# Kernel tuning notes

Hardware: AMD Instinct MI355X
Metric: run time of the kernel (lower is better)

Reference implementation:

```python
import jax, jax.numpy as jnp
import numpy as np

EPS = 1e-5
POOL_R, POOL_T, SCALE = 5, 7, 0.125  # pool_r, pool_t, 1/pool_stride


def conv_bn_relu(x, W, b, gamma, beta, pad):
    # Conv2d(bias) + BatchNorm2d (training-mode batch stats, biased var) + ReLU
    y = jax.lax.conv_general_dilated(x, W, (1, 1), [(pad, pad), (pad, pad)],
                                     dimension_numbers=('NCHW', 'OIHW', 'NCHW'))
    y = y + b[None, :, None, None]
    mean = y.mean(axis=(0, 2, 3))
    var = y.var(axis=(0, 2, 3))
    y = (y - mean[None, :, None, None]) * jax.lax.rsqrt(var + EPS)[None, :, None, None]
    y = y * gamma[None, :, None, None] + beta[None, :, None, None]
    return jax.nn.relu(y)


def linear_bn_relu(x, W, b, gamma, beta):
    # LinearBlock: Linear + BatchNorm (over batch dim) + ReLU
    y = x @ W.T + b
    mean = y.mean(axis=0)
    var = y.var(axis=0)
    y = (y - mean) * jax.lax.rsqrt(var + EPS) * gamma + beta
    return jax.nn.relu(y)


def _hat_int(x):
    # Antiderivative of the triangular (bilinear) hat kernel at offset x.
    u = jnp.clip(x, -1.0, 1.0)
    return jnp.where(u <= 0, 0.5 * (1.0 + u) ** 2, 0.5 + u - 0.5 * u ** 2)


def prroi_pool(feat, rois, ph, pw, scale):
    # Exact PrRoIPool2D. feat: [B,C,H,W]; rois: [B,N,4] xyxy in image coords.
    # Bilinear interp is a sum of separable hat kernels at integer grid points, so the
    # exact bin integral factorizes into per-axis hat-integral weights Wx, Wy.
    B, C, H, W = feat.shape
    x1, y1, x2, y2 = [rois[..., i] * scale for i in range(4)]
    bw = (x2 - x1) / pw   # [B,N]
    bh = (y2 - y1) / ph
    qx = jnp.arange(pw, dtype=feat.dtype)
    qy = jnp.arange(ph, dtype=feat.dtype)
    xs_lo = x1[..., None] + qx * bw[..., None]   # [B,N,Pw]
    ys_lo = y1[..., None] + qy * bh[..., None]   # [B,N,Ph]
    gw = jnp.arange(W, dtype=feat.dtype)
    gh = jnp.arange(H, dtype=feat.dtype)
    Wx = _hat_int(xs_lo[..., None] + bw[..., None, None] - gw) - _hat_int(xs_lo[..., None] - gw)  # [B,N,Pw,W]
    Wy = _hat_int(ys_lo[..., None] + bh[..., None, None] - gh) - _hat_int(ys_lo[..., None] - gh)  # [B,N,Ph,H]
    out = jnp.einsum('bchw,bnph,bnqw->bncpq', feat, Wy, Wx)
    area = (bw * bh)[:, :, None, None, None]
    return jnp.where(area > 0, out / jnp.maximum(area, 1e-12), 0.0)  # [B,N,C,Ph,Pw]


def _forward(feat1, feat2, bb1, proposals2,
             w_c1r, b_c1r, g_c1r, be_c1r,
             w_c1t, b_c1t, g_c1t, be_c1t,
             w_c2t, b_c2t, g_c2t, be_c2t,
             w_f1r, b_f1r, g_f1r, be_f1r,
             w_f2r, b_f2r, g_f2r, be_f2r,
             w_f1rt, b_f1rt, g_f1rt, be_f1rt,
             w_f2rt, b_f2rt, g_f2rt, be_f2rt,
             w_iou, b_iou):
    S = feat2.shape[0]
    N = proposals2.shape[2]
    # --- get_modulation ---
    c3_r = conv_bn_relu(feat1, w_c1r, b_c1r, g_c1r, be_c1r, 1)
    bb = bb1[0]  # [S,4] xywh -> xyxy
    roi_r = jnp.concatenate([bb[:, :2], bb[:, :2] + bb[:, 2:4]], axis=1)[:, None, :]
    pooled_r = prroi_pool(c3_r, roi_r, POOL_R, POOL_R, SCALE)[:, 0]   # [S,256,5,5]
    m = conv_bn_relu(pooled_r, w_f1r, b_f1r, g_f1r, be_f1r, 0)        # [S,1024,1,1]
    m = conv_bn_relu(m, w_f2r, b_f2r, g_f2r, be_f2r, 0)               # [S,256,1,1]
    modulation = m.reshape(S, -1)                                     # [S,256]
    # --- get_iou_feat ---
    c3_t = conv_bn_relu(conv_bn_relu(feat2, w_c1t, b_c1t, g_c1t, be_c1t, 1),
                        w_c2t, b_c2t, g_c2t, be_c2t, 1)
    # --- predict_iou ---
    c3_t_att = c3_t * modulation[:, :, None, None]
    props = proposals2[0]  # [S,N,4] xywh -> xyxy
    rois_t = jnp.concatenate([props[..., :2], props[..., :2] + props[..., 2:4]], axis=-1)
    pooled_t = prroi_pool(c3_t_att, rois_t, POOL_T, POOL_T, SCALE)    # [S,N,256,7,7]
    x = pooled_t.reshape(S * N, -1)
    x = linear_bn_relu(x, w_f1rt, b_f1rt, g_f1rt, be_f1rt)
    x = linear_bn_relu(x, w_f2rt, b_f2rt, g_f2rt, be_f2rt)
    iou = x @ w_iou.T + b_iou
    return iou.reshape(1, S, N)  # (num_images, num_sequences, num_proposals)


def setup_inputs() -> dict:
    key = jax.random.key(0)
    ks = jax.random.split(key, 8)
    S, C, Hf, Wf, N = 64, 256, 36, 36, 16
    inp = {}
    inp['feat1'] = jax.random.normal(ks[0], (S, C, Hf, Wf), jnp.float32)
    inp['feat2'] = jax.random.normal(ks[1], (S, C, Hf, Wf), jnp.float32)
    xy1 = jax.random.uniform(ks[2], (1, S, 2), minval=20.0, maxval=180.0)
    wh1 = jax.random.uniform(ks[3], (1, S, 2), minval=40.0, maxval=100.0)
    inp['bb1'] = jnp.concatenate([xy1, wh1], axis=-1).astype(jnp.float32)
    xy2 = jax.random.uniform(ks[4], (1, S, N, 2), minval=20.0, maxval=180.0)
    wh2 = jax.random.uniform(ks[5], (1, S, N, 2), minval=40.0, maxval=100.0)
    inp['proposals2'] = jnp.concatenate([xy2, wh2], axis=-1).astype(jnp.float32)

    def kaiming(k, shape):
        fan_in = int(np.prod(shape[1:]))
        return (jax.random.normal(k, shape) * np.sqrt(2.0 / fan_in)).astype(jnp.float32)

    kp = jax.random.split(ks[6], 8)
    specs = [('c1r', (256, C, 3, 3), kp[0]), ('c1t', (256, C, 3, 3), kp[1]),
             ('c2t', (256, 256, 3, 3), kp[2]), ('f1r', (1024, 256, 5, 5), kp[3]),
             ('f2r', (256, 1024, 1, 1), kp[4]), ('f1rt', (1024, 256 * 7 * 7), kp[5]),
             ('f2rt', (1024, 1024), kp[6])]
    for name, shape, k in specs:
        inp['w_' + name] = kaiming(k, shape)
        oc = shape[0]
        inp['b_' + name] = jnp.zeros(oc, jnp.float32)
        inp['g_' + name] = jnp.ones(oc, jnp.float32)
        inp['be_' + name] = jnp.zeros(oc, jnp.float32)
    inp['w_iou'] = kaiming(kp[7], (1, 1024))
    inp['b_iou'] = jnp.zeros(1, jnp.float32)
    return inp


def reference(feat1, feat2, bb1, proposals2,
              w_c1r, b_c1r, g_c1r, be_c1r,
              w_c1t, b_c1t, g_c1t, be_c1t,
              w_c2t, b_c2t, g_c2t, be_c2t,
              w_f1r, b_f1r, g_f1r, be_f1r,
              w_f2r, b_f2r, g_f2r, be_f2r,
              w_f1rt, b_f1rt, g_f1rt, be_f1rt,
              w_f2rt, b_f2rt, g_f2rt, be_f2rt,
              w_iou, b_iou):
    return _forward(feat1, feat2, bb1, proposals2,
                    w_c1r, b_c1r, g_c1r, be_c1r,
                    w_c1t, b_c1t, g_c1t, be_c1t,
                    w_c2t, b_c2t, g_c2t, be_c2t,
                    w_f1r, b_f1r, g_f1r, be_f1r,
                    w_f2r, b_f2r, g_f2r, be_f2r,
                    w_f1rt, b_f1rt, g_f1rt, be_f1rt,
                    w_f2rt, b_f2rt, g_f2rt, be_f2rt,
                    w_iou, b_iou)
```

## Files before the change

### kernel.cpp

```cpp
#include <hip/hip_runtime.h>
#include <cstddef>


typedef _Float16 f16;
typedef __attribute__((ext_vector_type(8))) _Float16 f16x8;
typedef __attribute__((ext_vector_type(4))) float f32x4;

__device__ __forceinline__ void gload16(const void* g, void* l) {
  __builtin_amdgcn_global_load_lds((const __attribute__((address_space(1))) void*)g,
                                   (__attribute__((address_space(3))) void*)l, 16, 0, 0);
}

#define WAITB(N) asm volatile("s_waitcnt vmcnt(" #N ")\n\ts_barrier" ::: "memory")
#define LGKB()   asm volatile("s_waitcnt lgkmcnt(0)\n\ts_barrier" ::: "memory")

static __device__ __forceinline__ float hat_int(float x) {
  float u = fminf(1.f, fmaxf(-1.f, x));
  float a = 0.5f * (1.f + u) * (1.f + u);
  float b = 0.5f + u - 0.5f * u * u;
  return (u <= 0.f) ? a : b;
}

static __device__ __forceinline__ size_t pk_off(int row, int k, int K) {
  return (size_t)(row >> 7) * ((size_t)K * 128) + (size_t)(k >> 5) * 4096
       + (size_t)((((k >> 3) & 3) * 128 + (row & 127)) * 8 + (k & 7));
}

__global__ void k_zero(float4* __restrict__ p, int n4) {
  int i = blockIdx.x * 256 + threadIdx.x;
  if (i < n4) p[i] = float4{0.f, 0.f, 0.f, 0.f};
}

__global__ void k_border(f16* __restrict__ FT) {
  const int img = blockIdx.x;
  f16* base = FT + (size_t)img * 32 * 1444 * 8;
  for (int i = threadIdx.x; i < 148 * 256; i += 256) {
    int b = i >> 8, c = i & 255;
    int r, cc;
    if (b < 38)       { r = 0;          cc = b; }
    else if (b < 76)  { r = 37;         cc = b - 38; }
    else if (b < 112) { r = b - 76 + 1; cc = 0; }
    else              { r = b - 112 + 1; cc = 37; }
    base[((size_t)(c >> 3) * 1444 + r * 38 + cc) * 8 + (c & 7)] = (f16)0.f;
  }
}

__global__ void k_pad(const float* __restrict__ src, f16* __restrict__ FT) {
  const int img = blockIdx.x, h = blockIdx.y, c = threadIdx.x;
  const float* sp = src + ((size_t)img * 256 + c) * 1296 + h * 36;
  f16* op = FT + (((size_t)img * 32 + (c >> 3)) * 1444 + (h + 1) * 38 + 1) * 8 + (c & 7);
#pragma unroll 4
  for (int w = 0; w < 36; ++w) op[w * 8] = (f16)sp[w];
}

__global__ void k_pad2(const f16* __restrict__ yH, f16* __restrict__ FT,
                       const float* __restrict__ mean, const float* __restrict__ istd,
                       const float* __restrict__ g, const float* __restrict__ be) {
  const int img = blockIdx.x, h = blockIdx.y, c = threadIdx.x;
  const float sc = istd[c] * g[c];
  const float sh = be[c] - mean[c] * sc;
  const f16* sp = yH + ((size_t)img * 1296 + h * 36) * 256 + c;
  f16* op = FT + (((size_t)img * 32 + (c >> 3)) * 1444 + (h + 1) * 38 + 1) * 8 + (c & 7);
#pragma unroll 4
  for (int w = 0; w < 36; ++w) {
    float v = fmaxf(fmaf((float)sp[w * 256], sc, sh), 0.f);
    op[w * 8] = (f16)v;
  }
}

__global__ void k_pack_wc(const float* __restrict__ w, f16* __restrict__ dst) {
  int i = blockIdx.x * 256 + threadIdx.x;
  int oct = i / 294912;
  int r = i - oct * 294912;
  int ks = r >> 12;
  int r2 = r & 4095;
  int koct = r2 >> 10;
  int r3 = r2 & 1023;
  int row = r3 >> 3, kj = r3 & 7;
  int k = ks * 32 + koct * 8 + kj;
  int t = k >> 8, c = k & 255;
  int oc = oct * 128 + row;
  dst[i] = (f16)w[(oc * 256 + c) * 9 + t];
}

__global__ __launch_bounds__(256) void k_packx_h(
    const f16* __restrict__ src, f16* __restrict__ dst, int M, int K) {
  __shared__ f16 sT[128][264];
  const int k0 = blockIdx.x * 256, r0 = blockIdx.y * 128;
  const int t = threadIdx.x;
  const int rl = t >> 5, kk = (t & 31) * 8;
  for (int rnd = 0; rnd < 16; ++rnd) {
    const int row_l = rl + rnd * 8;
    const int row = r0 + row_l;
    if (row < M) {
      f16x8 v = *reinterpret_cast<const f16x8*>(src + (size_t)row * K + k0 + kk);
      *reinterpret_cast<f16x8*>(&sT[row_l][kk]) = v;
    }
  }
  __syncthreads();
  const size_t base = (size_t)(r0 >> 7) * ((size_t)K * 128) + (size_t)(k0 >> 5) * 4096;
#pragma unroll
  for (int cs = 0; cs < 8; ++cs) {
#pragma unroll
    for (int half = 0; half < 2; ++half) {
      const int e = half * 256 + t;
      const int koct = e >> 7, row_l = e & 127;
      if (r0 + row_l < M) {
        f16x8 v = *reinterpret_cast<const f16x8*>(&sT[row_l][cs * 32 + koct * 8]);
        *reinterpret_cast<f16x8*>(dst + base + (size_t)cs * 4096 + e * 8) = v;
      }
    }
  }
}

__global__ __launch_bounds__(256) void k_packx_f(
    const float* __restrict__ src, f16* __restrict__ dst, int M, int K) {
  __shared__ f16 sT[128][264];
  const int k0 = blockIdx.x * 256, r0 = blockIdx.y * 128;
  const int t = threadIdx.x;
  const int rl = t >> 5, kk = (t & 31) * 8;
  for (int rnd = 0; rnd < 16; ++rnd) {
    const int row_l = rl + rnd * 8;
    const int row = r0 + row_l;
    if (row < M) {
      const float4* sp = reinterpret_cast<const float4*>(src + (size_t)row * K + k0 + kk);
      float4 a = sp[0], b = sp[1];
      f16* o = &sT[row_l][kk];
      o[0] = (f16)a.x; o[1] = (f16)a.y; o[2] = (f16)a.z; o[3] = (f16)a.w;
      o[4] = (f16)b.x; o[5] = (f16)b.y; o[6] = (f16)b.z; o[7] = (f16)b.w;
    }
  }
  __syncthreads();
  const size_t base = (size_t)(r0 >> 7) * ((size_t)K * 128) + (size_t)(k0 >> 5) * 4096;
#pragma unroll
  for (int cs = 0; cs < 8; ++cs) {
#pragma unroll
    for (int half = 0; half < 2; ++half) {
      const int e = half * 256 + t;
      const int koct = e >> 7, row_l = e & 127;
      if (r0 + row_l < M) {
        f16x8 v = *reinterpret_cast<const f16x8*>(&sT[row_l][cs * 32 + koct * 8]);
        *reinterpret_cast<f16x8*>(dst + base + (size_t)cs * 4096 + e * 8) = v;
      }
    }
  }
}

__global__ __launch_bounds__(256) void k_conv_mfma(
    const f16* __restrict__ Wpk, const f16* __restrict__ FT2,
    const float* __restrict__ bias, f16* __restrict__ yH) {
  __shared__ __align__(16) char smem[49152];
  f16x8* sA = (f16x8*)smem;
  f16x8* sB = (f16x8*)(smem + 24576);
  const int bid = blockIdx.x;
  const int orig = (bid & 7) * 176 + (bid >> 3);
  const int img = orig / 22;
  const int rem = orig - img * 22;
  const int oct = rem / 11;
  const int pt  = rem - oct * 11;
  const int m0 = oct * 128;
  const int p0 = pt * 128;
  const int tid = threadIdx.x;
  const int lane = tid & 63;
  const int wv = tid >> 6;
  const int wr = wv >> 1, wc = wv & 1;

  const f16* aBase = Wpk + (size_t)oct * 294912 + wv * 1024 + lane * 8;
  const f16* ftImg = FT2 + (size_t)img * 32 * 1444 * 8;
  int pos0 = p0 + lane;
  int pc0 = min(pos0, 1295);
  int pc1 = min(pos0 + 64, 1295);
  int pb0 = (pc0 / 36) * 38 + (pc0 % 36);
  int pb1 = (pc1 / 36) * 38 + (pc1 % 36);

  const int loff = wv * 2048 + lane * 16;

  auto stage = [&](int buf, int ks) {
    const int t = ks >> 3;
    const int dy = t / 3, dx = t - dy * 3;
    const int cs = ks & 7;
    const int dyx = dy * 38 + dx;
    char* lA = (char*)sA + buf * 8192 + loff;
    char* lB = (char*)sB + buf * 8192 + loff;
    const f16* ap = aBase + (size_t)ks * 4096;
    const f16* bp = ftImg + ((size_t)(cs * 4 + wv) * 1444 + dyx) * 8;
    gload16(ap, lA);
    gload16(ap + 512, lA + 1024);
    gload16(bp + pb0 * 8, lB);
    gload16(bp + pb1 * 8, lB + 1024);
  };

  f32x4 acc[4][4] = {};
  const int fidxA = ((lane >> 4) << 7) + wr * 64 + (lane & 15);
  const int fidxB = ((lane >> 4) << 7) + wc * 64 + (lane & 15);

  stage(0, 0); stage(1, 1); stage(2, 2);
  int cur = 0;
  for (int ks = 0; ks < 72; ++ks) {
    const int r = 71 - ks;
    if (r >= 2)      WAITB(8);
    else if (r == 1) WAITB(4);
    else             WAITB(0);
    const int base = cur * 512;
    f16x8 af[4], bf[4];
#pragma unroll
    for (int i = 0; i < 4; ++i) {
      af[i] = sA[base + fidxA + i * 16];
      bf[i] = sB[base + fidxB + i * 16];
    }
    __builtin_amdgcn_s_setprio(1);
#pragma unroll
    for (int i = 0; i < 4; ++i)
#pragma unroll
      for (int j = 0; j < 4; ++j)
        acc[i][j] = __builtin_amdgcn_mfma_f32_16x16x32_f16(af[i], bf[j], acc[i][j], 0, 0, 0);
    __builtin_amdgcn_s_setprio(0);
    LGKB();
    if (ks + 3 < 72) stage(cur, ks + 3);
    cur = (cur == 2) ? 0 : cur + 1;
  }

  __syncthreads();
  f16* sE = (f16*)smem;
  const int ocl = wr * 64 + ((lane >> 4) << 2);
#pragma unroll
  for (int i = 0; i < 4; ++i) {
    const int oc0 = m0 + ocl + i * 16;
    float b0 = bias[oc0], b1 = bias[oc0 + 1], b2 = bias[oc0 + 2], b3 = bias[oc0 + 3];
#pragma unroll
    for (int j = 0; j < 4; ++j) {
      f16* e = &sE[(wc * 64 + j * 16 + (lane & 15)) * 136 + ocl + i * 16];
      e[0] = (f16)(acc[i][j][0] + b0);
      e[1] = (f16)(acc[i][j][1] + b1);
      e[2] = (f16)(acc[i][j][2] + b2);
      e[3] = (f16)(acc[i][j][3] + b3);
    }
  }
  __syncthreads();
  f16* yb = yH + (size_t)img * 1296 * 256 + m0;
#pragma unroll
  for (int it = 0; it < 8; ++it) {
    const int e = (it * 256 + tid) * 8;
    const int row = e >> 7;
    const int oc = e & 127;
    const int col = p0 + row;
    if (col < 1296)
      *reinterpret_cast<f16x8*>(yb + (size_t)col * 256 + oc) =
        *reinterpret_cast<const f16x8*>(&sE[row * 136 + oc]);
  }
}

__global__ __launch_bounds__(256) void k_gemm_f16pk(
    const f16* __restrict__ Apk, const f16* __restrict__ Bpk,
    float* __restrict__ part, int K, int Nout, int stepsPerZ, int mrows) {
  __shared__ f16x8 sA[1536];
  __shared__ f16x8 sB[1536];
  const int nt = blockIdx.x, mt = blockIdx.y, z = blockIdx.z;
  const int tid = threadIdx.x;
  const int lane = tid & 63;
  const int wv = tid >> 6;
  const int wr = wv >> 1, wc = wv & 1;

  const f16* aC = Apk + (size_t)mt * K * 128 + wv * 1024 + lane * 8;
  const f16* bC = Bpk + (size_t)nt * K * 128 + wv * 1024 + lane * 8;
  const int loff = wv * 2048 + lane * 16;

  auto stage = [&](int buf, int ks) {
    char* lA = (char*)sA + buf * 8192 + loff;
    char* lB = (char*)sB + buf * 8192 + loff;
    const f16* ap = aC + (size_t)ks * 4096;
    const f16* bp = bC + (size_t)ks * 4096;
    gload16(ap, lA);
    gload16(ap + 512, lA + 1024);
    gload16(bp, lB);
    gload16(bp + 512, lB + 1024);
  };

  f32x4 acc[4][4] = {};
  const int fidxA = ((lane >> 4) << 7) + wr * 64 + (lane & 15);
  const int fidxB = ((lane >> 4) << 7) + wc * 64 + (lane & 15);

  const int ks0 = z * stepsPerZ;
  stage(0, ks0); stage(1, ks0 + 1); stage(2, ks0 + 2);
  int cur = 0;
  for (int i = 0; i < stepsPerZ; ++i) {
    const int r = stepsPerZ - 1 - i;
    if (r >= 2)      WAITB(8);
    else if (r == 1) WAITB(4);
    else             WAITB(0);
    const int base = cur * 512;
    f16x8 af[4], bf[4];
#pragma unroll
    for (int j = 0; j < 4; ++j) {
      af[j] = sA[base + fidxA + j * 16];
      bf[j] = sB[base + fidxB + j * 16];
    }
    __builtin_amdgcn_s_setprio(1);
#pragma unroll
    for (int ii = 0; ii < 4; ++ii)
#pragma unroll
      for (int jj = 0; jj < 4; ++jj)
        acc[ii][jj] = __builtin_amdgcn_mfma_f32_16x16x32_f16(af[ii], bf[jj], acc[ii][jj], 0, 0, 0);
    __builtin_amdgcn_s_setprio(0);
    LGKB();
    if (i + 3 < stepsPerZ) stage(cur, ks0 + i + 3);
    cur = (cur == 2) ? 0 : cur + 1;
  }

  const size_t zoff = (size_t)z * mrows * Nout;
  const int colb = nt * 128 + wc * 64 + (lane & 15);
  const int rowb = mt * 128 + wr * 64 + ((lane >> 4) << 2);
#pragma unroll
  for (int i = 0; i < 4; ++i)
#pragma unroll
    for (int j = 0; j < 4; ++j)
#pragma unroll
      for (int r = 0; r < 4; ++r)
        part[zoff + (size_t)(rowb + i * 16 + r) * Nout + colb + j * 16] = acc[i][j][r];
}

__global__ void k_reduce_stats(const float* __restrict__ part, const float* __restrict__ bias,
                               float* __restrict__ out, int mrows, int Mout, int Nout,
                               int sk, int rpz,
                               float* __restrict__ psum, float* __restrict__ psq) {
  const int col = blockIdx.x * 256 + threadIdx.x;
  const int z = blockIdx.y;
  const float b = bias[col];
  float s = 0.f, ss = 0.f;
  const int r0 = z * rpz, r1 = min(Mout, r0 + rpz);
  for (int m = r0; m < r1; ++m) {
    float v = b;
    for (int zz = 0; zz < sk; ++zz)
      v += part[(size_t)zz * mrows * Nout + (size_t)m * Nout + col];
    out[(size_t)m * Nout + col] = v;
    s += v; ss += v * v;
  }
  psum[(size_t)z * Nout + col] = s;
  psq[(size_t)z * Nout + col] = ss;
}

__global__ void k_chan_stats_hwc(const f16* __restrict__ yH,
                                 float* __restrict__ psum, float* __restrict__ psq) {
  const int z = blockIdx.x, c = threadIdx.x;
  const f16* p = yH + (size_t)z * 256 * 256 + c;
  float s = 0.f, ss = 0.f;
#pragma unroll 4
  for (int i = 0; i < 256; ++i) {
    float v = (float)p[(size_t)i * 256];
    s += v; ss += v * v;
  }
  psum[z * 256 + c] = s;
  psq[z * 256 + c] = ss;
}

__global__ void k_chan_stats_hwc_final(const float* __restrict__ psum,
                                       const float* __restrict__ psq,
                                       float* __restrict__ mean, float* __restrict__ istd) {
  const int c = threadIdx.x;
  float s = 0.f, ss = 0.f;
  for (int z = 0; z < 324; ++z) { s += psum[z * 256 + c]; ss += psq[z * 256 + c]; }
  float m = s * (1.f / 82944.f);
  float var = ss * (1.f / 82944.f) - m * m;
  mean[c] = m;
  istd[c] = rsqrtf(var + 1e-5f);
}

__global__ void k_wxy(const float* __restrict__ rois, int ntot, int P,
                      float* __restrict__ Wx, float* __restrict__ Wy,
                      float* __restrict__ area,
                      int* __restrict__ HLO, int* __restrict__ HCNT,
                      int* __restrict__ WLO) {
  int idx = blockIdx.x * blockDim.x + threadIdx.x;
  if (idx >= ntot) return;
  float rx = rois[idx * 4 + 0], ry = rois[idx * 4 + 1];
  float rw = rois[idx * 4 + 2], rh = rois[idx * 4 + 3];
  float x1 = rx * 0.125f, y1 = ry * 0.125f;
  float x2 = (rx + rw) * 0.125f, y2 = (ry + rh) * 0.125f;
  float bw = (x2 - x1) / P, bh = (y2 - y1) / P;
  area[idx] = bw * bh;
  int hlo = max(0, (int)ceilf(y1 - 1.f));
  int hhi = min(35, (int)floorf(y2 + 1.f));
  HLO[idx] = hlo;
  HCNT[idx] = max(0, hhi - hlo + 1);
  for (int q = 0; q < P; ++q) {
    float xlo = x1 + q * bw, ylo = y1 + q * bh;
    WLO[idx * P + q] = min(31, max(0, (int)ceilf(xlo - 1.f)));
    for (int g = 0; g < 36; ++g) {
      float fg = (float)g;
      Wx[(idx * P + q) * 36 + g] = hat_int(xlo + bw - fg) - hat_int(xlo - fg);
      Wy[(idx * P + q) * 36 + g] = hat_int(ylo + bh - fg) - hat_int(ylo - fg);
    }
  }
}

template <int P, bool MOD>
__global__ __launch_bounds__(256) void k_pool(
    const f16* __restrict__ feat, const float* __restrict__ Wx,
    const float* __restrict__ Wy, const float* __restrict__ area,
    const int* __restrict__ HLO, const int* __restrict__ HCNT,
    const int* __restrict__ WLO,
    const float* __restrict__ mean, const float* __restrict__ istd,
    const float* __restrict__ g, const float* __restrict__ be,
    const float* __restrict__ mod, f16* __restrict__ out, int N) {
  const int s = blockIdx.x, n = blockIdx.y;
  const int idx = s * N + n;
  const int c = threadIdx.x;
  constexpr int KD = P * P * 256;
  __shared__ f16 sOut[KD];
  __shared__ float sWx[P * 36], sWy[P * 36];
  __shared__ int sWLO[P];
  __shared__ int sH[2];
  for (int i = threadIdx.x; i < P * 36; i += 256) {
    sWx[i] = Wx[(size_t)idx * P * 36 + i];
    sWy[i] = Wy[(size_t)idx * P * 36 + i];
  }
  if (threadIdx.x < P) sWLO[threadIdx.x] = WLO[idx * P + threadIdx.x];
  if (threadIdx.x == 0) { sH[0] = HLO[idx]; sH[1] = HCNT[idx]; }
  __syncthreads();
  const float sc = istd[c] * g[c];
  const float sh = be[c] - mean[c] * sc;
  const f16* f = feat + (size_t)s * 1296 * 256 + c;
  float o[P][P] = {};
  const int hlo = sH[0], hcnt = sH[1];
  for (int hh = 0; hh < hcnt; ++hh) {
    const int h = hlo + hh;
    const f16* rp = f + (size_t)h * 36 * 256;
    float colsum[P];
#pragma unroll
    for (int q = 0; q < P; ++q) {
      const int w0 = sWLO[q];
      const f16* wp = rp + (size_t)w0 * 256;
      float v = 0.f;
#pragma unroll
      for (int j = 0; j < 5; ++j) {
        float x = fmaxf(fmaf((float)wp[j * 256], sc, sh), 0.f);
        v = fmaf(sWx[q * 36 + w0 + j], x, v);
      }
      colsum[q] = v;
    }
#pragma unroll
    for (int p = 0; p < P; ++p) {
      const float wy = sWy[p * 36 + h];
      if (wy != 0.f) {
#pragma unroll
        for (int q = 0; q < P; ++q) o[p][q] = fmaf(wy, colsum[q], o[p][q]);
      }
    }
  }
  float a = area[idx];
  float inv = (a > 0.f) ? 1.f / fmaxf(a, 1e-12f) : 0.f;
  float msc = MOD ? (mod[s * 256 + c] * inv) : inv;
  const int kbase = c * (P * P);
#pragma unroll
  for (int p = 0; p < P; ++p)
#pragma unroll
    for (int q = 0; q < P; ++q)
      sOut[kbase + p * P + q] = (f16)(o[p][q] * msc);
  __syncthreads();
  f16* op = out + (size_t)idx * KD;
  for (int j = threadIdx.x; j < KD; j += 256) op[j] = sOut[j];
}

__global__ void k_fc_stats_final(const float* __restrict__ psum, const float* __restrict__ psq,
                                 int nz, int Nf, int M,
                                 float* __restrict__ mean, float* __restrict__ istd) {
  int col = blockIdx.x * 256 + threadIdx.x;
  if (col >= Nf) return;
  float s = 0.f, ss = 0.f;
  for (int z = 0; z < nz; ++z) {
    s += psum[(size_t)z * Nf + col];
    ss += psq[(size_t)z * Nf + col];
  }
  float mu = s / (float)M;
  float var = ss / (float)M - mu * mu;
  mean[col] = mu;
  istd[col] = rsqrtf(var + 1e-5f);
}

__global__ void k_fc_bn_relu(float* __restrict__ y, const float* __restrict__ mean,
                             const float* __restrict__ istd, const float* __restrict__ g,
                             const float* __restrict__ be, int total, int Nf) {
  int i = blockIdx.x * 256 + threadIdx.x;
  if (i >= total) return;
  int col = i % Nf;
  float sc = istd[col] * g[col];
  float sh = be[col] - mean[col] * sc;
  y[i] = fmaxf(fmaf(y[i], sc, sh), 0.f);
}

__global__ void k_fc_bn_relu_pk(const float* __restrict__ y, const float* __restrict__ mean,
                                const float* __restrict__ istd, const float* __restrict__ g,
                                const float* __restrict__ be, f16* __restrict__ xpk,
                                int total, int Nf) {
  int i = blockIdx.x * 256 + threadIdx.x;
  if (i >= total) return;
  int row = i / Nf, col = i - row * Nf;
  float sc = istd[col] * g[col];
  float sh = be[col] - mean[col] * sc;
  float v = fmaxf(fmaf(y[i], sc, sh), 0.f);
  xpk[pk_off(row, col, Nf)] = (f16)v;
}

__global__ void k_iou(const float* __restrict__ x, const float* __restrict__ w,
                      const float* __restrict__ b, float* __restrict__ out) {
  const int r = blockIdx.x, tid = threadIdx.x;
  float s = 0.f;
  for (int k = tid; k < 1024; k += 256) s = fmaf(x[(size_t)r * 1024 + k], w[k], s);
  __shared__ float red[256];
  red[tid] = s;
  __syncthreads();
  for (int o = 128; o > 0; o >>= 1) {
    if (tid < o) red[tid] += red[tid + o];
    __syncthreads();
  }
  if (tid == 0) out[r] = red[0] + b[0];
}

static const size_t O_A      = 0;
static const size_t O_POOLT  = 12000000;
static const size_t O_PSUM   = 13000000;
static const size_t O_PSQ    = 13065536;
static const size_t O_WPK2RT = 16000000;
static const size_t O_POOLR  = 18500000;
static const size_t O_WPK2R  = 20000000;
static const size_t O_FT     = 21233664;
static const size_t O_X2PK   = 21233664 + 6422528;
static const size_t O_WC     = 33062912;
static const size_t O_WPK1RT = 33357824;
static const size_t O_WPK1R  = 39780352;
static const size_t O_PRPK   = 43057152;
static const size_t O_Y1     = 43466752;
static const size_t O_Y2     = 44515328;
static const size_t O_MOD    = 45563904;
static const size_t O_WXR    = 45580288;
static const size_t O_WYR    = 45591808;
static const size_t O_ARR    = 45603328;
static const size_t O_WXT    = 45603392;
static const size_t O_WYT    = 45861440;
static const size_t O_ART    = 46119488;
static const size_t O_MEAN   = 46120512;
static const size_t O_ISTD   = 46121536;
static const size_t O_X1PK   = 46122560;
static const size_t O_META   = 46188096;
static const size_t O_PSC    = 46197760;

extern "C" void kernel_launch(void* const* d_in, const int* in_sizes, int n_in,
                              void* d_out, int out_size, void* d_ws, size_t ws_size,
                              hipStream_t stream) {
  (void)in_sizes; (void)n_in; (void)out_size; (void)ws_size;
  const float* feat1  = (const float*)d_in[0];
  const float* feat2  = (const float*)d_in[1];
  const float* bb1    = (const float*)d_in[2];
  const float* props  = (const float*)d_in[3];
  const float* w_c1r  = (const float*)d_in[4];
  const float* b_c1r  = (const float*)d_in[5];
  const float* g_c1r  = (const float*)d_in[6];
  const float* be_c1r = (const float*)d_in[7];
  const float* w_c1t  = (const float*)d_in[8];
  const float* b_c1t  = (const float*)d_in[9];
  const float* g_c1t  = (const float*)d_in[10];
  const float* be_c1t = (const float*)d_in[11];
  const float* w_c2t  = (const float*)d_in[12];
  const float* b_c2t  = (const float*)d_in[13];
  const float* g_c2t  = (const float*)d_in[14];
  const float* be_c2t = (const float*)d_in[15];
  const float* w_f1r  = (const float*)d_in[16];
  const float* b_f1r  = (const float*)d_in[17];
  const float* g_f1r  = (const float*)d_in[18];
  const float* be_f1r = (const float*)d_in[19];
  const float* w_f2r  = (const float*)d_in[20];
  const float* b_f2r  = (const float*)d_in[21];
  const float* g_f2r  = (const float*)d_in[22];
  const float* be_f2r = (const float*)d_in[23];
  const float* w_f1rt = (const float*)d_in[24];
  const float* b_f1rt = (const float*)d_in[25];
  const float* g_f1rt = (const float*)d_in[26];
  const float* be_f1rt= (const float*)d_in[27];
  const float* w_f2rt = (const float*)d_in[28];
  const float* b_f2rt = (const float*)d_in[29];
  const float* g_f2rt = (const float*)d_in[30];
  const float* be_f2rt= (const float*)d_in[31];
  const float* w_iou  = (const float*)d_in[32];
  const float* b_iou  = (const float*)d_in[33];

  float* ws    = (float*)d_ws;
  f16*   AH    = (f16*)(ws + O_A);
  float* PART  = ws + O_A;
  f16*   POOLT = (f16*)(ws + O_POOLT);
  float* PSUM  = ws + O_PSUM;
  float* PSQ   = ws + O_PSQ;
  f16*   WPK2RT= (f16*)(ws + O_WPK2RT);
  f16*   POOLR = (f16*)(ws + O_POOLR);
  f16*   WPK2R = (f16*)(ws + O_WPK2R);
  f16*   FT2   = (f16*)(ws + O_FT);
  f16*   PHPK  = FT2;
  f16*   X2PK  = (f16*)(ws + O_X2PK);
  f16*   WC    = (f16*)(ws + O_WC);
  f16*   WPK1RT= (f16*)(ws + O_WPK1RT);
  f16*   WPK1R = (f16*)(ws + O_WPK1R);
  f16*   PRPK  = (f16*)(ws + O_PRPK);
  float* Y1    = ws + O_Y1;
  float* Y2    = ws + O_Y2;
  float* MODp  = ws + O_MOD;
  float* WXR   = ws + O_WXR;
  float* WYR   = ws + O_WYR;
  float* ARR   = ws + O_ARR;
  float* WXT   = ws + O_WXT;
  float* WYT   = ws + O_WYT;
  float* ART   = ws + O_ART;
  float* MEAN  = ws + O_MEAN;
  float* ISTD  = ws + O_ISTD;
  f16*   X1PK  = (f16*)(ws + O_X1PK);
  int*   META  = (int*)(ws + O_META);
  float* PSUMC = ws + O_PSC;
  float* PSQC  = ws + O_PSC + 82944;
  int* HLOR = META;
  int* HCNTR= META + 64;
  int* WLOR = META + 128;
  int* HLOT = META + 448;
  int* HCNTT= META + 1472;
  int* WLOT = META + 2496;

  k_border<<<64, 256, 0, stream>>>(FT2);
  k_pack_wc<<<2304, 256, 0, stream>>>(w_c1r, WC);
  k_pad<<<dim3(64, 36), 256, 0, stream>>>(feat1, FT2);
  k_conv_mfma<<<1408, 256, 0, stream>>>(WC, FT2, b_c1r, AH);
  k_chan_stats_hwc<<<324, 256, 0, stream>>>(AH, PSUMC, PSQC);
  k_chan_stats_hwc_final<<<1, 256, 0, stream>>>(PSUMC, PSQC, MEAN, ISTD);

  k_wxy<<<1, 64, 0, stream>>>(bb1, 64, 5, WXR, WYR, ARR, HLOR, HCNTR, WLOR);
  k_zero<<<400, 256, 0, stream>>>((float4*)PRPK, 102400);
  k_pool<5, false><<<dim3(64, 1), 256, 0, stream>>>(
      AH, WXR, WYR, ARR, HLOR, HCNTR, WLOR, MEAN, ISTD, g_c1r, be_c1r, nullptr, POOLR, 1);
  k_packx_h<<<dim3(25, 1), 256, 0, stream>>>(POOLR, PRPK, 64, 6400);

  k_packx_f<<<dim3(25, 8), 256, 0, stream>>>(w_f1r, WPK1R, 1024, 6400);
  k_gemm_f16pk<<<dim3(8, 1, 8), 256, 0, stream>>>(PRPK, WPK1R, PART, 6400, 1024, 25, 128);
  k_reduce_stats<<<dim3(4, 8), 256, 0, stream>>>(PART, b_f1r, Y1, 128, 64, 1024, 8, 8, PSUM, PSQ);
  k_fc_stats_final<<<4, 256, 0, stream>>>(PSUM, PSQ, 8, 1024, 64, MEAN, ISTD);
  k_zero<<<64, 256, 0, stream>>>((float4*)X1PK, 16384);
  k_fc_bn_relu_pk<<<256, 256, 0, stream>>>(Y1, MEAN, ISTD, g_f1r, be_f1r, X1PK, 64 * 1024, 1024);

  k_packx_f<<<dim3(4, 2), 256, 0, stream>>>(w_f2r, WPK2R, 256, 1024);
  k_gemm_f16pk<<<dim3(2, 1, 4), 256, 0, stream>>>(X1PK, WPK2R, PART, 1024, 256, 8, 128);
  k_reduce_stats<<<dim3(1, 8), 256, 0, stream>>>(PART, b_f2r, MODp, 128, 64, 256, 4, 8, PSUM, PSQ);
  k_fc_stats_final<<<1, 256, 0, stream>>>(PSUM, PSQ, 8, 256, 64, MEAN, ISTD);
  k_fc_bn_relu<<<64, 256, 0, stream>>>(MODp, MEAN, ISTD, g_f2r, be_f2r, 64 * 256, 256);

  k_pack_wc<<<2304, 256, 0, stream>>>(w_c1t, WC);
  k_pad<<<dim3(64, 36), 256, 0, stream>>>(feat2, FT2);
  k_conv_mfma<<<1408, 256, 0, stream>>>(WC, FT2, b_c1t, AH);
  k_chan_stats_hwc<<<324, 256, 0, stream>>>(AH, PSUMC, PSQC);
  k_chan_stats_hwc_final<<<1, 256, 0, stream>>>(PSUMC, PSQC, MEAN, ISTD);
  k_pad2<<<dim3(64, 36), 256, 0, stream>>>(AH, FT2, MEAN, ISTD, g_c1t, be_c1t);

  k_pack_wc<<<2304, 256, 0, stream>>>(w_c2t, WC);
  k_conv_mfma<<<1408, 256, 0, stream>>>(WC, FT2, b_c2t, AH);
  k_chan_stats_hwc<<<324, 256, 0, stream>>>(AH, PSUMC, PSQC);
  k_chan_stats_hwc_final<<<1, 256, 0, stream>>>(PSUMC, PSQC, MEAN, ISTD);

  k_wxy<<<16, 64, 0, stream>>>(props, 1024, 7, WXT, WYT, ART, HLOT, HCNTT, WLOT);
  k_pool<7, true><<<dim3(64, 16), 256, 0, stream>>>(
      AH, WXT, WYT, ART, HLOT, HCNTT, WLOT, MEAN, ISTD, g_c2t, be_c2t, MODp, POOLT, 16);
  k_packx_h<<<dim3(49, 8), 256, 0, stream>>>(POOLT, PHPK, 1024, 12544);

  k_packx_f<<<dim3(49, 8), 256, 0, stream>>>(w_f1rt, WPK1RT, 1024, 12544);
  k_gemm_f16pk<<<dim3(8, 8, 8), 256, 0, stream>>>(PHPK, WPK1RT, PART, 12544, 1024, 49, 1024);
  k_reduce_stats<<<dim3(4, 64), 256, 0, stream>>>(PART, b_f1rt, Y1, 1024, 1024, 1024, 8, 16, PSUM, PSQ);
  k_fc_stats_final<<<4, 256, 0, stream>>>(PSUM, PSQ, 64, 1024, 1024, MEAN, ISTD);
  k_fc_bn_relu_pk<<<4096, 256, 0, stream>>>(Y1, MEAN, ISTD, g_f1rt, be_f1rt, X2PK, 1024 * 1024, 1024);

  k_packx_f<<<dim3(4, 8), 256, 0, stream>>>(w_f2rt, WPK2RT, 1024, 1024);
  k_gemm_f16pk<<<dim3(8, 8, 4), 256, 0, stream>>>(X2PK, WPK2RT, PART, 1024, 1024, 8, 1024);
  k_reduce_stats<<<dim3(4, 64), 256, 0, stream>>>(PART, b_f2rt, Y2, 1024, 1024, 1024, 4, 16, PSUM, PSQ);
  k_fc_stats_final<<<4, 256, 0, stream>>>(PSUM, PSQ, 64, 1024, 1024, MEAN, ISTD);
  k_fc_bn_relu<<<4096, 256, 0, stream>>>(Y2, MEAN, ISTD, g_f2rt, be_f2rt, 1024 * 1024, 1024);

  k_iou<<<1024, 256, 0, stream>>>(Y2, w_iou, b_iou, (float*)d_out);
}
```

Baseline: 974.3 us.

## Fuse BN channel stats into conv epilogue and transpose-pad via shared memory

Per-channel sum and sum-of-squares are now computed in the conv kernel epilogue from the shared-memory output tile. This replaces a separate stats pass over the conv output and folds partials in two small kernels. The pad and border kernels are merged into one that stages 8 channels in LDS and writes 16-byte vectors. FC stat reductions also use more row partitions for more parallelism. The risk is an epilogue loop run by only half the threads, which lengthens the conv tail.

```diff
diff --git a/kernel.cpp b/kernel.cpp
--- a/kernel.cpp
+++ b/kernel.cpp
@@ -31,26 +31,33 @@
   if (i < n4) p[i] = float4{0.f, 0.f, 0.f, 0.f};
 }
 
-__global__ void k_border(f16* __restrict__ FT) {
-  const int img = blockIdx.x;
-  f16* base = FT + (size_t)img * 32 * 1444 * 8;
-  for (int i = threadIdx.x; i < 148 * 256; i += 256) {
-    int b = i >> 8, c = i & 255;
+__global__ __launch_bounds__(256) void k_padT(const float* __restrict__ src,
+                                              f16* __restrict__ FT) {
+  __shared__ f16 sT[8][1300];
+  const int img = blockIdx.x, kk = blockIdx.y;
+  const float* sp = src + ((size_t)img * 256 + kk * 8) * 1296;
+#pragma unroll
+  for (int c = 0; c < 8; ++c)
+    for (int i = threadIdx.x; i < 1296; i += 256)
+      sT[c][i] = (f16)sp[c * 1296 + i];
+  __syncthreads();
+  f16* op = FT + ((size_t)img * 32 + kk) * 1444 * 8;
+  for (int i = threadIdx.x; i < 148; i += 256) {
     int r, cc;
-    if (b < 38)       { r = 0;          cc = b; }
-    else if (b < 76)  { r = 37;         cc = b - 38; }
-    else if (b < 112) { r = b - 76 + 1; cc = 0; }
-    else              { r = b - 112 + 1; cc = 37; }
-    base[((size_t)(c >> 3) * 1444 + r * 38 + cc) * 8 + (c & 7)] = (f16)0.f;
-  }
-}
-
-__global__ void k_pad(const float* __restrict__ src, f16* __restrict__ FT) {
-  const int img = blockIdx.x, h = blockIdx.y, c = threadIdx.x;
-  const float* sp = src + ((size_t)img * 256 + c) * 1296 + h * 36;
-  f16* op = FT + (((size_t)img * 32 + (c >> 3)) * 1444 + (h + 1) * 38 + 1) * 8 + (c & 7);
-#pragma unroll 4
-  for (int w = 0; w < 36; ++w) op[w * 8] = (f16)sp[w];
+    if (i < 38)       { r = 0;          cc = i; }
+    else if (i < 76)  { r = 37;         cc = i - 38; }
+    else if (i < 112) { r = i - 76 + 1; cc = 0; }
+    else              { r = i - 112 + 1; cc = 37; }
+    f16x8 z = {};
+    *reinterpret_cast<f16x8*>(op + (r * 38 + cc) * 8) = z;
+  }
+  for (int i = threadIdx.x; i < 1296; i += 256) {
+    const int h = i / 36, w = i - h * 36;
+    f16x8 v;
+#pragma unroll
+    for (int c = 0; c < 8; ++c) v[c] = sT[c][i];
+    *reinterpret_cast<f16x8*>(op + ((h + 1) * 38 + w + 1) * 8) = v;
+  }
 }
 
 __global__ void k_pad2(const f16* __restrict__ yH, f16* __restrict__ FT,
@@ -148,7 +155,8 @@
 
 __global__ __launch_bounds__(256) void k_conv_mfma(
     const f16* __restrict__ Wpk, const f16* __restrict__ FT2,
-    const float* __restrict__ bias, f16* __restrict__ yH) {
+    const float* __restrict__ bias, f16* __restrict__ yH,
+    float* __restrict__ psc) {
   __shared__ __align__(16) char smem[49152];
   f16x8* sA = (f16x8*)smem;
   f16x8* sB = (f16x8*)(smem + 24576);
@@ -248,6 +256,40 @@
       *reinterpret_cast<f16x8*>(yb + (size_t)col * 256 + oc) =
         *reinterpret_cast<const f16x8*>(&sE[row * 136 + oc]);
   }
+  const int nvalid = min(128, 1296 - p0);
+  if (tid < 128) {
+    float s = 0.f, ss = 0.f;
+    for (int row = 0; row < nvalid; ++row) {
+      float v = (float)sE[row * 136 + tid];
+      s += v; ss += v * v;
+    }
+    const int bi = (img * 11 + pt) * 256 + m0 + tid;
+    psc[bi] = s;
+    psc[180224 + bi] = ss;
+  }
+}
+
+__global__ void k_chan_fold8(const float* __restrict__ psc, float* __restrict__ out2) {
+  const int z = blockIdx.x, c = threadIdx.x;
+  float s = 0.f, ss = 0.f;
+  for (int i = z * 88; i < z * 88 + 88; ++i) {
+    s += psc[i * 256 + c];
+    ss += psc[180224 + i * 256 + c];
+  }
+  out2[z * 256 + c] = s;
+  out2[2048 + z * 256 + c] = ss;
+}
+
+__global__ void k_chan_final2(const float* __restrict__ out2,
+                              float* __restrict__ mean, float* __restrict__ istd) {
+  const int c = threadIdx.x;
+  float s = 0.f, ss = 0.f;
+#pragma unroll
+  for (int z = 0; z < 8; ++z) { s += out2[z * 256 + c]; ss += out2[2048 + z * 256 + c]; }
+  float m = s * (1.f / 82944.f);
+  float var = ss * (1.f / 82944.f) - m * m;
+  mean[c] = m;
+  istd[c] = rsqrtf(var + 1e-5f);
 }
 
 __global__ __launch_bounds__(256) void k_gemm_f16pk(
@@ -337,32 +379,6 @@
   }
   psum[(size_t)z * Nout + col] = s;
   psq[(size_t)z * Nout + col] = ss;
-}
-
-__global__ void k_chan_stats_hwc(const f16* __restrict__ yH,
-                                 float* __restrict__ psum, float* __restrict__ psq) {
-  const int z = blockIdx.x, c = threadIdx.x;
-  const f16* p = yH + (size_t)z * 256 * 256 + c;
-  float s = 0.f, ss = 0.f;
-#pragma unroll 4
-  for (int i = 0; i < 256; ++i) {
-    float v = (float)p[(size_t)i * 256];
-    s += v; ss += v * v;
-  }
-  psum[z * 256 + c] = s;
-  psq[z * 256 + c] = ss;
-}
-
-__global__ void k_chan_stats_hwc_final(const float* __restrict__ psum,
-                                       const float* __restrict__ psq,
-                                       float* __restrict__ mean, float* __restrict__ istd) {
-  const int c = threadIdx.x;
-  float s = 0.f, ss = 0.f;
-  for (int z = 0; z < 324; ++z) { s += psum[z * 256 + c]; ss += psq[z * 256 + c]; }
-  float m = s * (1.f / 82944.f);
-  float var = ss * (1.f / 82944.f) - m * m;
-  mean[c] = m;
-  istd[c] = rsqrtf(var + 1e-5f);
 }
 
 __global__ void k_wxy(const float* __restrict__ rois, int ntot, int P,
@@ -518,8 +534,10 @@
 
 static const size_t O_A      = 0;
 static const size_t O_POOLT  = 12000000;
+static const size_t O_PSC2   = 12000000;
+static const size_t O_PSC2B  = 12400000;
 static const size_t O_PSUM   = 13000000;
-static const size_t O_PSQ    = 13065536;
+static const size_t O_PSQ    = 13200000;
 static const size_t O_WPK2RT = 16000000;
 static const size_t O_POOLR  = 18500000;
 static const size_t O_WPK2R  = 20000000;
@@ -542,7 +560,6 @@
 static const size_t O_ISTD   = 46121536;
 static const size_t O_X1PK   = 46122560;
 static const size_t O_META   = 46188096;
-static const size_t O_PSC    = 46197760;
 
 extern "C" void kernel_launch(void* const* d_in, const int* in_sizes, int n_in,
                               void* d_out, int out_size, void* d_ws, size_t ws_size,
@@ -587,6 +604,8 @@
   f16*   AH    = (f16*)(ws + O_A);
   float* PART  = ws + O_A;
   f16*   POOLT = (f16*)(ws + O_POOLT);
+  float* PSC2  = ws + O_PSC2;
+  float* PSC2B = ws + O_PSC2B;
   float* PSUM  = ws + O_PSUM;
   float* PSQ   = ws + O_PSQ;
   f16*   WPK2RT= (f16*)(ws + O_WPK2RT);
@@ -612,8 +631,6 @@
   float* ISTD  = ws + O_ISTD;
   f16*   X1PK  = (f16*)(ws + O_X1PK);
   int*   META  = (int*)(ws + O_META);
-  float* PSUMC = ws + O_PSC;
-  float* PSQC  = ws + O_PSC + 82944;
   int* HLOR = META;
   int* HCNTR= META + 64;
   int* WLOR = META + 128;
@@ -621,12 +638,11 @@
   int* HCNTT= META + 1472;
   int* WLOT = META + 2496;
 
-  k_border<<<64, 256, 0, stream>>>(FT2);
   k_pack_wc<<<2304, 256, 0, stream>>>(w_c1r, WC);
-  k_pad<<<dim3(64, 36), 256, 0, stream>>>(feat1, FT2);
-  k_conv_mfma<<<1408, 256, 0, stream>>>(WC, FT2, b_c1r, AH);
-  k_chan_stats_hwc<<<324, 256, 0, stream>>>(AH, PSUMC, PSQC);
-  k_chan_stats_hwc_final<<<1, 256, 0, stream>>>(PSUMC, PSQC, MEAN, ISTD);
+  k_padT<<<dim3(64, 32), 256, 0, stream>>>(feat1, FT2);
+  k_conv_mfma<<<1408, 256, 0, stream>>>(WC, FT2, b_c1r, AH, PSC2);
+  k_chan_fold8<<<8, 256, 0, stream>>>(PSC2, PSC2B);
+  k_chan_final2<<<1, 256, 0, stream>>>(PSC2B, MEAN, ISTD);
 
   k_wxy<<<1, 64, 0, stream>>>(bb1, 64, 5, WXR, WYR, ARR, HLOR, HCNTR, WLOR);
   k_zero<<<400, 256, 0, stream>>>((float4*)PRPK, 102400);
@@ -648,16 +664,16 @@
   k_fc_bn_relu<<<64, 256, 0, stream>>>(MODp, MEAN, ISTD, g_f2r, be_f2r, 64 * 256, 256);
 
   k_pack_wc<<<2304, 256, 0, stream>>>(w_c1t, WC);
-  k_pad<<<dim3(64, 36), 256, 0, stream>>>(feat2, FT2);
-  k_conv_mfma<<<1408, 256, 0, stream>>>(WC, FT2, b_c1t, AH);
-  k_chan_stats_hwc<<<324, 256, 0, stream>>>(AH, PSUMC, PSQC);
-  k_chan_stats_hwc_final<<<1, 256, 0, stream>>>(PSUMC, PSQC, MEAN, ISTD);
+  k_padT<<<dim3(64, 32), 256, 0, stream>>>(feat2, FT2);
+  k_conv_mfma<<<1408, 256, 0, stream>>>(WC, FT2, b_c1t, AH, PSC2);
+  k_chan_fold8<<<8, 256, 0, stream>>>(PSC2, PSC2B);
+  k_chan_final2<<<1, 256, 0, stream>>>(PSC2B, MEAN, ISTD);
   k_pad2<<<dim3(64, 36), 256, 0, stream>>>(AH, FT2, MEAN, ISTD, g_c1t, be_c1t);
 
   k_pack_wc<<<2304, 256, 0, stream>>>(w_c2t, WC);
-  k_conv_mfma<<<1408, 256, 0, stream>>>(WC, FT2, b_c2t, AH);
-  k_chan_stats_hwc<<<324, 256, 0, stream>>>(AH, PSUMC, PSQC);
-  k_chan_stats_hwc_final<<<1, 256, 0, stream>>>(PSUMC, PSQC, MEAN, ISTD);
+  k_conv_mfma<<<1408, 256, 0, stream>>>(WC, FT2, b_c2t, AH, PSC2);
+  k_chan_fold8<<<8, 256, 0, stream>>>(PSC2, PSC2B);
+  k_chan_final2<<<1, 256, 0, stream>>>(PSC2B, MEAN, ISTD);
 
   k_wxy<<<16, 64, 0, stream>>>(props, 1024, 7, WXT, WYT, ART, HLOT, HCNTT, WLOT);
   k_pool<7, true><<<dim3(64, 16), 256, 0, stream>>>(
@@ -666,14 +682,14 @@
 
   k_packx_f<<<dim3(49, 8), 256, 0, stream>>>(w_f1rt, WPK1RT, 1024, 12544);
   k_gemm_f16pk<<<dim3(8, 8, 8), 256, 0, stream>>>(PHPK, WPK1RT, PART, 12544, 1024, 49, 1024);
-  k_reduce_stats<<<dim3(4, 64), 256, 0, stream>>>(PART, b_f1rt, Y1, 1024, 1024, 1024, 8, 16, PSUM, PSQ);
-  k_fc_stats_final<<<4, 256, 0, stream>>>(PSUM, PSQ, 64, 1024, 1024, MEAN, ISTD);
+  k_reduce_stats<<<dim3(4, 128), 256, 0, stream>>>(PART, b_f1rt, Y1, 1024, 1024, 1024, 8, 8, PSUM, PSQ);
+  k_fc_stats_final<<<4, 256, 0, stream>>>(PSUM, PSQ, 128, 1024, 1024, MEAN, ISTD);
   k_fc_bn_relu_pk<<<4096, 256, 0, stream>>>(Y1, MEAN, ISTD, g_f1rt, be_f1rt, X2PK, 1024 * 1024, 1024);
 
   k_packx_f<<<dim3(4, 8), 256, 0, stream>>>(w_f2rt, WPK2RT, 1024, 1024);
   k_gemm_f16pk<<<dim3(8, 8, 4), 256, 0, stream>>>(X2PK, WPK2RT, PART, 1024, 1024, 8, 1024);
-  k_reduce_stats<<<dim3(4, 64), 256, 0, stream>>>(PART, b_f2rt, Y2, 1024, 1024, 1024, 4, 16, PSUM, PSQ);
-  k_fc_stats_final<<<4, 256, 0, stream>>>(PSUM, PSQ, 64, 1024, 1024, MEAN, ISTD);
+  k_reduce_stats<<<dim3(4, 128), 256, 0, stream>>>(PART, b_f2rt, Y2, 1024, 1024, 1024, 4, 8, PSUM, PSQ);
+  k_fc_stats_final<<<4, 256, 0, stream>>>(PSUM, PSQ, 128, 1024, 1024, MEAN, ISTD);
   k_fc_bn_relu<<<4096, 256, 0, stream>>>(Y2, MEAN, ISTD, g_f2rt, be_f2rt, 1024 * 1024, 1024);
 
   k_iou<<<1024, 256, 0, stream>>>(Y2, w_iou, b_iou, (float*)d_out);
```

New measurement: 893.7 us. 1.09x faster.
